# Kernel optimization log

Hardware: AMD Instinct MI355X
Metric: run time of the kernel (lower is better)

## Reference

```python
import jax, jax.numpy as jnp
import numpy as np

B, T, D_MODEL, H, D = 2, 2048, 1024, 16, 64
EPS = 1e-5


def _layernorm(x, g, b):
    m = jnp.mean(x, axis=-1, keepdims=True)
    v = jnp.var(x, axis=-1, keepdims=True)
    return (x - m) * jax.lax.rsqrt(v + EPS) * g + b


def setup_inputs() -> dict:
    key = jax.random.key(0)
    ks = jax.random.split(key, 5)
    qab = H * D
    x = jax.random.normal(ks[0], (B, T, D_MODEL), dtype=jnp.float32)
    sc = 1.0 / np.sqrt(D_MODEL)
    Wq = jax.random.normal(ks[1], (D_MODEL, qab), dtype=jnp.float32) * sc
    Wa = jax.random.normal(ks[2], (D_MODEL, qab), dtype=jnp.float32) * sc
    Wb = jax.random.normal(ks[3], (D_MODEL, qab), dtype=jnp.float32) * sc
    Wo = jax.random.normal(ks[4], (qab, D_MODEL), dtype=jnp.float32) * (1.0 / np.sqrt(qab))
    g = jnp.ones((D,), dtype=jnp.float32)
    z = jnp.zeros((D,), dtype=jnp.float32)
    return {"x": x, "Wq": Wq, "Wa": Wa, "Wb": Wb, "Wo": Wo,
            "q_gamma": g, "q_beta": z, "a_gamma": g, "a_beta": z,
            "b_gamma": g, "b_beta": z}


def reference(x, Wq, Wa, Wb, Wo, q_gamma, q_beta, a_gamma, a_beta, b_gamma, b_beta):
    def split_heads(y):  # (B,T,H*D) -> (B,H,T,D)
        Bx, Tx, _ = y.shape
        return y.reshape(Bx, Tx, H, D).transpose(0, 2, 1, 3)

    q = _layernorm(split_heads(x @ Wq), q_gamma, q_beta)
    a = _layernorm(split_heads(x @ Wa), a_gamma, a_beta)
    b = _layernorm(split_heads(x @ Wb), b_gamma, b_beta)

    # strict-exclusive cumsum of a along time
    a_excl = jnp.cumsum(a, axis=-2) - a
    # o_t = q_t . sum_{j<=t} a_excl_j (x) b_j  ==  causal (q a_excl^T) b
    scores = jnp.einsum('bhtd,bhsd->bhts', q, a_excl)  # (B,H,T,T)
    causal = jnp.tril(jnp.ones((T, T), dtype=scores.dtype))  # j <= t
    o = jnp.einsum('bhts,bhse->bhte', scores * causal, b)  # (B,H,T,D)

    o = o.transpose(0, 2, 1, 3).reshape(B, T, H * D)  # merge heads
    return o @ Wo
```

## Files before the change

kernel.cpp:

```cpp
#include <hip/hip_runtime.h>
#include <hip/hip_bf16.h>

#define T_LEN  2048
#define NHEAD  16
#define HDIM   64
#define DMODEL 1024
#define BATCH  2
#define MROWS  4096
#define L_CHK  64
#define N_CHK  (T_LEN / L_CHK)
#define BH     (BATCH * NHEAD)

typedef __attribute__((ext_vector_type(8))) short short8;
typedef __attribute__((ext_vector_type(4))) float f32x4;
typedef __attribute__((ext_vector_type(4))) unsigned short ushort4v;

#define GLDS(GP, LP) __builtin_amdgcn_global_load_lds( \
    (__attribute__((address_space(1))) void*)(void*)(GP), \
    (__attribute__((address_space(3))) void*)(LP), 16, 0, 0)

__device__ __forceinline__ unsigned short f2bf(float f) {
  union { float f; unsigned int u; } v; v.f = f;
  unsigned int r = v.u + 0x7FFFu + ((v.u >> 16) & 1u);
  return (unsigned short)(r >> 16);
}
__device__ __forceinline__ float bf2f(short s) {
  union { unsigned int u; float f; } v;
  v.u = ((unsigned int)(unsigned short)s) << 16;
  return v.f;
}

__global__ __launch_bounds__(256) void ha_convx(
    const float* __restrict__ X, short* __restrict__ Xb) {
  const size_t idx = (size_t)(blockIdx.x * 256 + threadIdx.x) * 8;
  float4 v0 = *(const float4*)(X + idx);
  float4 v1 = *(const float4*)(X + idx + 4);
  short8 o;
  o[0] = (short)f2bf(v0.x); o[1] = (short)f2bf(v0.y);
  o[2] = (short)f2bf(v0.z); o[3] = (short)f2bf(v0.w);
  o[4] = (short)f2bf(v1.x); o[5] = (short)f2bf(v1.y);
  o[6] = (short)f2bf(v1.z); o[7] = (short)f2bf(v1.w);
  *(short8*)(Xb + idx) = o;
}

__global__ __launch_bounds__(256) void ha_convT4(
    const float* __restrict__ Wq, const float* __restrict__ Wa,
    const float* __restrict__ Wb, const float* __restrict__ Wo,
    short* __restrict__ wqabT, short* __restrict__ woT) {
  __shared__ float tile[64][65];
  const int z = blockIdx.z;
  const float* W = (z == 0) ? Wq : (z == 1) ? Wa : (z == 2) ? Wb : Wo;
  short* WT = (z < 3) ? wqabT + (size_t)z * 1024 * DMODEL : woT;
  const int k0 = blockIdx.y * 64, n0 = blockIdx.x * 64;
  const int tid = threadIdx.x;
  #pragma unroll
  for (int p = 0; p < 4; ++p) {
    const int r  = p * 16 + (tid >> 4);
    const int c4 = (tid & 15) * 4;
    float4 v = *(const float4*)(W + (size_t)(k0 + r) * DMODEL + n0 + c4);
    tile[r][c4 + 0] = v.x; tile[r][c4 + 1] = v.y;
    tile[r][c4 + 2] = v.z; tile[r][c4 + 3] = v.w;
  }
  __syncthreads();
  #pragma unroll
  for (int p = 0; p < 4; ++p) {
    const int n = p * 16 + (tid >> 4);
    const int c = (tid & 15) * 4;
    ushort4v o = { f2bf(tile[c + 0][n]), f2bf(tile[c + 1][n]),
                   f2bf(tile[c + 2][n]), f2bf(tile[c + 3][n]) };
    *(ushort4v*)(WT + (size_t)(n0 + n) * DMODEL + k0 + c) = o;
  }
}

__global__ __launch_bounds__(256) void ha_gemm_qab(
    const short* __restrict__ Ab, const short* __restrict__ Bt,
    short* __restrict__ q, short* __restrict__ a, short* __restrict__ bOut,
    const float* __restrict__ qg, const float* __restrict__ qbet,
    const float* __restrict__ ag, const float* __restrict__ abet,
    const float* __restrict__ bg, const float* __restrict__ bbet) {
  __shared__ short As[128 * 32] __attribute__((aligned(16)));
  __shared__ short Bs[128 * 32] __attribute__((aligned(16)));
  const int tid = threadIdx.x;
  const int wave = tid >> 6, lane = tid & 63;
  const int m0  = blockIdx.y * 128;
  const int n0g = blockIdx.x * 128;
  short* Cbuf; const float* gamma; const float* beta;
  if (n0g < 1024)      { Cbuf = q;    gamma = qg; beta = qbet; }
  else if (n0g < 2048) { Cbuf = a;    gamma = ag; beta = abet; }
  else                 { Cbuf = bOut; gamma = bg; beta = bbet; }
  const int n0 = n0g & 1023;

  const int srow = wave * 32 + (lane >> 2);
  const int scol = (lane & 3) * 8;
  const short* agp = Ab + (size_t)(m0 + srow) * DMODEL + scol;
  const short* bgp = Bt + (size_t)(n0g + srow) * DMODEL + scol;
  short* alp = As + wave * 32 * 32;
  short* blp = Bs + wave * 32 * 32;

  f32x4 acc[4][4] = {};
  const int lm = lane & 15, kh = lane >> 4;
  const int wm = (wave >> 1) * 64, wn = (wave & 1) * 64;

  float gl[4], bl[4];
  #pragma unroll
  for (int j = 0; j < 4; ++j) {
    gl[j] = gamma[j * 16 + lm];
    bl[j] = beta[j * 16 + lm];
  }

  for (int k0 = 0; k0 < DMODEL; k0 += 32) {
    GLDS(agp,               alp);
    GLDS(agp + 16 * DMODEL, alp + 16 * 32);
    GLDS(bgp,               blp);
    GLDS(bgp + 16 * DMODEL, blp + 16 * 32);
    agp += 32; bgp += 32;
    __syncthreads();
    short8 af[4], bf[4];
    #pragma unroll
    for (int i = 0; i < 4; ++i) {
      af[i] = *(const short8*)&As[(wm + i * 16 + lm) * 32 + kh * 8];
      bf[i] = *(const short8*)&Bs[(wn + i * 16 + lm) * 32 + kh * 8];
    }
    #pragma unroll
    for (int i = 0; i < 4; ++i)
      #pragma unroll
      for (int j = 0; j < 4; ++j)
        acc[i][j] = __builtin_amdgcn_mfma_f32_16x16x32_bf16(
            af[i], bf[j], acc[i][j], 0, 0, 0);
    __syncthreads();
  }

  #pragma unroll
  for (int i = 0; i < 4; ++i) {
    float s1[4] = {0.f, 0.f, 0.f, 0.f};
    float s2[4] = {0.f, 0.f, 0.f, 0.f};
    #pragma unroll
    for (int j = 0; j < 4; ++j)
      #pragma unroll
      for (int r = 0; r < 4; ++r) {
        const float v = acc[i][j][r];
        s1[r] += v; s2[r] += v * v;
      }
    #pragma unroll
    for (int m = 1; m <= 8; m <<= 1)
      #pragma unroll
      for (int r = 0; r < 4; ++r) {
        s1[r] += __shfl_xor(s1[r], m);
        s2[r] += __shfl_xor(s2[r], m);
      }
    #pragma unroll
    for (int r = 0; r < 4; ++r) {
      const float mean = s1[r] * 0.015625f;
      const float var  = s2[r] * 0.015625f - mean * mean;
      const float rs   = rsqrtf(var + 1e-5f);
      short* cp = Cbuf + (size_t)(m0 + wm + i * 16 + kh * 4 + r) * DMODEL +
                  n0 + wn + lm;
      #pragma unroll
      for (int j = 0; j < 4; ++j)
        cp[j * 16] = (short)f2bf((acc[i][j][r] - mean) * rs * gl[j] + bl[j]);
    }
  }
}

__global__ __launch_bounds__(256) void ha_gemm_out(
    const short* __restrict__ Ab, const short* __restrict__ Bt,
    float* __restrict__ C) {
  __shared__ short As[128 * 32] __attribute__((aligned(16)));
  __shared__ short Bs[64 * 32] __attribute__((aligned(16)));
  const int tid = threadIdx.x;
  const int wave = tid >> 6, lane = tid & 63;
  const int m0 = blockIdx.y * 128;
  const int n0 = blockIdx.x * 64;

  const int arow = wave * 32 + (lane >> 2);
  const int brow = wave * 16 + (lane >> 2);
  const int scol = (lane & 3) * 8;
  const short* agp = Ab + (size_t)(m0 + arow) * DMODEL + scol;
  const short* bgp = Bt + (size_t)(n0 + brow) * DMODEL + scol;
  short* alp = As + wave * 32 * 32;
  short* blp = Bs + wave * 16 * 32;

  f32x4 acc[4][2] = {};
  const int lm = lane & 15, kh = lane >> 4;
  const int wm = (wave >> 1) * 64, wn = (wave & 1) * 32;

  for (int k0 = 0; k0 < DMODEL; k0 += 32) {
    GLDS(agp,               alp);
    GLDS(agp + 16 * DMODEL, alp + 16 * 32);
    GLDS(bgp,               blp);
    agp += 32; bgp += 32;
    __syncthreads();
    short8 af[4], bf2[2];
    #pragma unroll
    for (int i = 0; i < 4; ++i)
      af[i] = *(const short8*)&As[(wm + i * 16 + lm) * 32 + kh * 8];
    #pragma unroll
    for (int j = 0; j < 2; ++j)
      bf2[j] = *(const short8*)&Bs[(wn + j * 16 + lm) * 32 + kh * 8];
    #pragma unroll
    for (int i = 0; i < 4; ++i)
      #pragma unroll
      for (int j = 0; j < 2; ++j)
        acc[i][j] = __builtin_amdgcn_mfma_f32_16x16x32_bf16(
            af[i], bf2[j], acc[i][j], 0, 0, 0);
    __syncthreads();
  }
  #pragma unroll
  for (int i = 0; i < 4; ++i)
    #pragma unroll
    for (int j = 0; j < 2; ++j) {
      float* cp = C + (size_t)(m0 + wm + i * 16 + kh * 4) * DMODEL +
                  n0 + wn + j * 16 + lm;
      #pragma unroll
      for (int r = 0; r < 4; ++r) cp[(size_t)r * DMODEL] = acc[i][j][r];
    }
}

__global__ __launch_bounds__(256) void ha_scan1(
    const short* __restrict__ An, const short* __restrict__ Bn,
    float* __restrict__ M, float* __restrict__ Asums, float* __restrict__ Bsums) {
  __shared__ float Al[64][68];
  __shared__ float Bl[64][68];
  __shared__ float sega[4][64];
  __shared__ float segb[4][64];
  const int bid = blockIdx.x;
  const int c   = bid & (N_CHK - 1);
  const int bh  = bid >> 5;
  const int b = bh >> 4, h = bh & 15;
  const int tid = threadIdx.x;
  const size_t rowbase = ((size_t)b * T_LEN + (size_t)c * L_CHK) * DMODEL + h * HDIM;

  #pragma unroll
  for (int i = 0; i < 2; ++i) {
    const int idx = tid + 256 * i;
    const int s = idx >> 3, c8 = (idx & 7) * 8;
    short8 a8 = *(const short8*)(An + rowbase + (size_t)s * DMODEL + c8);
    short8 b8 = *(const short8*)(Bn + rowbase + (size_t)s * DMODEL + c8);
    #pragma unroll
    for (int k = 0; k < 8; ++k) {
      Al[s][c8 + k] = bf2f(a8[k]);
      Bl[s][c8 + k] = bf2f(b8[k]);
    }
  }
  __syncthreads();

  const int d = tid & 63, seg = tid >> 6;
  {
    float run = 0.f, runb = 0.f;
    for (int s = seg * 16; s < seg * 16 + 16; ++s) {
      const float va = Al[s][d];
      Al[s][d] = run;
      run  += va;
      runb += Bl[s][d];
    }
    sega[seg][d] = run;
    segb[seg][d] = runb;
  }
  __syncthreads();
  {
    float off = 0.f;
    for (int qq = 0; qq < seg; ++qq) off += sega[qq][d];
    for (int s = seg * 16; s < seg * 16 + 16; ++s) Al[s][d] += off;
    if (seg == 0) {
      Asums[((size_t)bh * N_CHK + c) * 64 + d] =
          sega[0][d] + sega[1][d] + sega[2][d] + sega[3][d];
      Bsums[((size_t)bh * N_CHK + c) * 64 + d] =
          segb[0][d] + segb[1][d] + segb[2][d] + segb[3][d];
    }
  }
  __syncthreads();

  const int e0 = (tid >> 4) * 4, d0 = (tid & 15) * 4;
  float acc[4][4];
  #pragma unroll
  for (int i = 0; i < 4; ++i)
    #pragma unroll
    for (int j = 0; j < 4; ++j) acc[i][j] = 0.f;
  #pragma unroll 8
  for (int s = 0; s < 64; ++s) {
    const float4 bv = *(const float4*)&Bl[s][e0];
    const float4 av = *(const float4*)&Al[s][d0];
    const float bb_[4] = {bv.x, bv.y, bv.z, bv.w};
    const float aa_[4] = {av.x, av.y, av.z, av.w};
    #pragma unroll
    for (int i = 0; i < 4; ++i)
      #pragma unroll
      for (int j = 0; j < 4; ++j) acc[i][j] = fmaf(bb_[i], aa_[j], acc[i][j]);
  }
  float* Mp = M + ((size_t)bh * N_CHK + c) * 4096;
  #pragma unroll
  for (int i = 0; i < 4; ++i)
    *(float4*)(Mp + (e0 + i) * 64 + d0) =
        make_float4(acc[i][0], acc[i][1], acc[i][2], acc[i][3]);
}

__global__ __launch_bounds__(64) void ha_aoff(float* __restrict__ Asums) {
  const int bh = blockIdx.x, d = threadIdx.x;
  float run = 0.f;
  for (int c = 0; c < N_CHK; ++c) {
    const size_t off = ((size_t)bh * N_CHK + c) * 64 + d;
    const float v = Asums[off];
    Asums[off] = run;
    run += v;
  }
}

__global__ __launch_bounds__(256) void ha_s2p(
    float* __restrict__ M, const float* __restrict__ Aoff,
    const float* __restrict__ Bsums) {
  const int part = blockIdx.x & 7;
  const int bh   = blockIdx.x >> 3;
  const int tid  = threadIdx.x;
  const int e = part * 8 + (tid >> 5);
  const int d = (tid & 31) * 2;
  float2 S = make_float2(0.f, 0.f);
  for (int c = 0; c < N_CHK; ++c) {
    const size_t vec = ((size_t)bh * N_CHK + c) * 64;
    const float bs = Bsums[vec + e];
    const float2 ao = *(const float2*)&Aoff[vec + d];
    float* Mp = M + ((size_t)bh * N_CHK + c) * 4096 + e * 64 + d;
    const float2 m = *(const float2*)Mp;
    *(float2*)Mp = S;
    S.x += fmaf(bs, ao.x, m.x);
    S.y += fmaf(bs, ao.y, m.y);
  }
}

__global__ __launch_bounds__(256) void ha_scan3(
    const short* __restrict__ Qn, const short* __restrict__ An,
    const short* __restrict__ Bn, const float* __restrict__ Soff,
    const float* __restrict__ Aoff, short* __restrict__ Ob) {
  __shared__ float Qt[64][68];
  __shared__ float Gt[64][68];
  __shared__ float Bl[64][68];
  __shared__ float Pt[64][68];
  const int bid = blockIdx.x;
  const int c   = bid & (N_CHK - 1);
  const int bh  = bid >> 5;
  const int b = bh >> 4, h = bh & 15;
  const int tid = threadIdx.x;
  const size_t rowbase = ((size_t)b * T_LEN + (size_t)c * L_CHK) * DMODEL + h * HDIM;

  #pragma unroll
  for (int i = 0; i < 2; ++i) {
    const int idx = tid + 256 * i;
    const int t = idx >> 3, c8 = (idx & 7) * 8;
    short8 q8 = *(const short8*)(Qn + rowbase + (size_t)t * DMODEL + c8);
    short8 a8 = *(const short8*)(An + rowbase + (size_t)t * DMODEL + c8);
    short8 b8 = *(const short8*)(Bn + rowbase + (size_t)t * DMODEL + c8);
    #pragma unroll
    for (int k = 0; k < 8; ++k) {
      Qt[c8 + k][t] = bf2f(q8[k]);
      Gt[c8 + k][t] = bf2f(a8[k]);
      Bl[t][c8 + k] = bf2f(b8[k]);
    }
  }
  __syncthreads();

  if (tid < 64) {
    float run = Aoff[((size_t)bh * N_CHK + c) * 64 + tid];
    for (int s = 0; s < 64; ++s) {
      const float v = Gt[tid][s];
      Gt[tid][s] = run;
      run += v;
    }
  }
  __syncthreads();

  const int tt = tid >> 4, ss = tid & 15;
  const int t0 = tt * 4, s0 = ss * 4;
  {
    float p[4][4];
    #pragma unroll
    for (int i = 0; i < 4; ++i)
      #pragma unroll
      for (int j = 0; j < 4; ++j) p[i][j] = 0.f;
    #pragma unroll 8
    for (int k = 0; k < 64; ++k) {
      const float4 qv = *(const float4*)&Qt[k][t0];
      const float4 gv = *(const float4*)&Gt[k][s0];
      const float qq[4] = {qv.x, qv.y, qv.z, qv.w};
      const float gg[4] = {gv.x, gv.y, gv.z, gv.w};
      #pragma unroll
      for (int i = 0; i < 4; ++i)
        #pragma unroll
        for (int j = 0; j < 4; ++j) p[i][j] = fmaf(qq[i], gg[j], p[i][j]);
    }
    #pragma unroll
    for (int i = 0; i < 4; ++i)
      #pragma unroll
      for (int j = 0; j < 4; ++j)
        Pt[s0 + j][t0 + i] = (s0 + j <= t0 + i) ? p[i][j] : 0.f;
  }
  __syncthreads();

  const float* Sg = Soff + ((size_t)bh * N_CHK + c) * 4096;
  #pragma unroll
  for (int i = 0; i < 4; ++i) {
    const int idx = tid + 256 * i;
    const int e = idx >> 4, d4 = idx & 15;
    float4 s4 = *(const float4*)(Sg + (size_t)e * 64 + d4 * 4);
    Gt[d4 * 4 + 0][e] = s4.x; Gt[d4 * 4 + 1][e] = s4.y;
    Gt[d4 * 4 + 2][e] = s4.z; Gt[d4 * 4 + 3][e] = s4.w;
  }
  __syncthreads();

  const int e0 = s0;
  float o[4][4];
  #pragma unroll
  for (int i = 0; i < 4; ++i)
    #pragma unroll
    for (int j = 0; j < 4; ++j) o[i][j] = 0.f;
  #pragma unroll 8
  for (int s = 0; s < 64; ++s) {
    const float4 pv = *(const float4*)&Pt[s][t0];
    const float4 bv = *(const float4*)&Bl[s][e0];
    const float pp[4] = {pv.x, pv.y, pv.z, pv.w};
    const float bb_[4] = {bv.x, bv.y, bv.z, bv.w};
    #pragma unroll
    for (int i = 0; i < 4; ++i)
      #pragma unroll
      for (int j = 0; j < 4; ++j) o[i][j] = fmaf(pp[i], bb_[j], o[i][j]);
  }
  #pragma unroll 8
  for (int dd = 0; dd < 64; ++dd) {
    const float4 qv = *(const float4*)&Qt[dd][t0];
    const float4 sv = *(const float4*)&Gt[dd][e0];
    const float qq[4] = {qv.x, qv.y, qv.z, qv.w};
    const float sS[4] = {sv.x, sv.y, sv.z, sv.w};
    #pragma unroll
    for (int i = 0; i < 4; ++i)
      #pragma unroll
      for (int j = 0; j < 4; ++j) o[i][j] = fmaf(qq[i], sS[j], o[i][j]);
  }
  #pragma unroll
  for (int i = 0; i < 4; ++i) {
    ushort4v o4 = { f2bf(o[i][0]), f2bf(o[i][1]), f2bf(o[i][2]), f2bf(o[i][3]) };
    *(ushort4v*)(Ob + rowbase + (size_t)(t0 + i) * DMODEL + e0) = o4;
  }
}

extern "C" void kernel_launch(void* const* d_in, const int* in_sizes, int n_in,
                              void* d_out, int out_size, void* d_ws,
                              size_t ws_size, hipStream_t stream) {
  const float* x  = (const float*)d_in[0];
  const float* Wq = (const float*)d_in[1];
  const float* Wa = (const float*)d_in[2];
  const float* Wb = (const float*)d_in[3];
  const float* Wo = (const float*)d_in[4];
  const float* qg = (const float*)d_in[5];
  const float* qb = (const float*)d_in[6];
  const float* ag = (const float*)d_in[7];
  const float* ab = (const float*)d_in[8];
  const float* bg = (const float*)d_in[9];
  const float* bb = (const float*)d_in[10];
  float* out = (float*)d_out;

  char* ws = (char*)d_ws;
  short* qn  = (short*)(ws);
  short* an  = (short*)(ws + ((size_t)8  << 20));
  short* bn  = (short*)(ws + ((size_t)16 << 20));
  short* xb  = (short*)(ws + ((size_t)24 << 20));
  short* obb = xb;
  short* wqabT = (short*)(ws + ((size_t)32 << 20));
  short* woT   = (short*)(ws + ((size_t)38 << 20));
  float* asums = (float*)(ws + ((size_t)40 << 20));
  float* bsums = asums + (size_t)BH * N_CHK * 64;
  float* Mbuf  = out;

  ha_convx<<<(MROWS * DMODEL) / (256 * 8), 256, 0, stream>>>(x, xb);
  ha_convT4<<<dim3(16, 16, 4), 256, 0, stream>>>(Wq, Wa, Wb, Wo, wqabT, woT);

  ha_gemm_qab<<<dim3(24, 32), 256, 0, stream>>>(xb, wqabT, qn, an, bn,
                                                qg, qb, ag, ab, bg, bb);

  ha_scan1<<<BH * N_CHK, 256, 0, stream>>>(an, bn, Mbuf, asums, bsums);
  ha_aoff<<<BH, 64, 0, stream>>>(asums);
  ha_s2p<<<BH * 8, 256, 0, stream>>>(Mbuf, asums, bsums);
  ha_scan3<<<BH * N_CHK, 256, 0, stream>>>(qn, an, bn, Mbuf, asums, obb);

  ha_gemm_out<<<dim3(16, 32), 256, 0, stream>>>(obb, woT, out);
}
```

Before: 205.2 us.

## Merge conversion and prefix kernels, XOR-swizzle GEMM LDS tiles

Folds the x-to-bf16 conversion into the weight-transpose launch as an extra grid slice. Folds the chunk-offset prefix scan into the state-propagation kernel: each block recomputes the prefix in LDS and one block per head writes it out. Adds an XOR swizzle to the LDS column layout of both GEMMs to cut bank conflicts on fragment reads. This removes two launches and some LDS contention, at the cost of redundant prefix work across 8 blocks per head and one extra workspace buffer.

```diff
diff --git a/kernel.cpp b/kernel.cpp
--- a/kernel.cpp
+++ b/kernel.cpp
@@ -30,29 +30,34 @@
   return v.f;
 }
 
-__global__ __launch_bounds__(256) void ha_convx(
-    const float* __restrict__ X, short* __restrict__ Xb) {
-  const size_t idx = (size_t)(blockIdx.x * 256 + threadIdx.x) * 8;
-  float4 v0 = *(const float4*)(X + idx);
-  float4 v1 = *(const float4*)(X + idx + 4);
-  short8 o;
-  o[0] = (short)f2bf(v0.x); o[1] = (short)f2bf(v0.y);
-  o[2] = (short)f2bf(v0.z); o[3] = (short)f2bf(v0.w);
-  o[4] = (short)f2bf(v1.x); o[5] = (short)f2bf(v1.y);
-  o[6] = (short)f2bf(v1.z); o[7] = (short)f2bf(v1.w);
-  *(short8*)(Xb + idx) = o;
-}
-
-__global__ __launch_bounds__(256) void ha_convT4(
+__global__ __launch_bounds__(256) void ha_conv(
     const float* __restrict__ Wq, const float* __restrict__ Wa,
     const float* __restrict__ Wb, const float* __restrict__ Wo,
-    short* __restrict__ wqabT, short* __restrict__ woT) {
+    const float* __restrict__ X,
+    short* __restrict__ wqabT, short* __restrict__ woT,
+    short* __restrict__ Xb) {
+  const int z = blockIdx.z;
+  const int tid = threadIdx.x;
+  if (z == 4) {
+    const int bidl = blockIdx.y * 16 + blockIdx.x;
+    #pragma unroll
+    for (int p = 0; p < 8; ++p) {
+      const size_t idx = (size_t)bidl * 16384 + (size_t)p * 2048 + tid * 8;
+      float4 v0 = *(const float4*)(X + idx);
+      float4 v1 = *(const float4*)(X + idx + 4);
+      short8 o;
+      o[0] = (short)f2bf(v0.x); o[1] = (short)f2bf(v0.y);
+      o[2] = (short)f2bf(v0.z); o[3] = (short)f2bf(v0.w);
+      o[4] = (short)f2bf(v1.x); o[5] = (short)f2bf(v1.y);
+      o[6] = (short)f2bf(v1.z); o[7] = (short)f2bf(v1.w);
+      *(short8*)(Xb + idx) = o;
+    }
+    return;
+  }
   __shared__ float tile[64][65];
-  const int z = blockIdx.z;
   const float* W = (z == 0) ? Wq : (z == 1) ? Wa : (z == 2) ? Wb : Wo;
   short* WT = (z < 3) ? wqabT + (size_t)z * 1024 * DMODEL : woT;
   const int k0 = blockIdx.y * 64, n0 = blockIdx.x * 64;
-  const int tid = threadIdx.x;
   #pragma unroll
   for (int p = 0; p < 4; ++p) {
     const int r  = p * 16 + (tid >> 4);
@@ -91,7 +96,7 @@
   const int n0 = n0g & 1023;
 
   const int srow = wave * 32 + (lane >> 2);
-  const int scol = (lane & 3) * 8;
+  const int scol = (((lane & 3) ^ ((lane >> 3) & 3))) * 8;
   const short* agp = Ab + (size_t)(m0 + srow) * DMODEL + scol;
   const short* bgp = Bt + (size_t)(n0g + srow) * DMODEL + scol;
   short* alp = As + wave * 32 * 32;
@@ -100,6 +105,7 @@
   f32x4 acc[4][4] = {};
   const int lm = lane & 15, kh = lane >> 4;
   const int wm = (wave >> 1) * 64, wn = (wave & 1) * 64;
+  const int khs = (kh ^ ((lm >> 1) & 3)) * 8;
 
   float gl[4], bl[4];
   #pragma unroll
@@ -118,8 +124,8 @@
     short8 af[4], bf[4];
     #pragma unroll
     for (int i = 0; i < 4; ++i) {
-      af[i] = *(const short8*)&As[(wm + i * 16 + lm) * 32 + kh * 8];
-      bf[i] = *(const short8*)&Bs[(wn + i * 16 + lm) * 32 + kh * 8];
+      af[i] = *(const short8*)&As[(wm + i * 16 + lm) * 32 + khs];
+      bf[i] = *(const short8*)&Bs[(wn + i * 16 + lm) * 32 + khs];
     }
     #pragma unroll
     for (int i = 0; i < 4; ++i)
@@ -174,7 +180,7 @@
 
   const int arow = wave * 32 + (lane >> 2);
   const int brow = wave * 16 + (lane >> 2);
-  const int scol = (lane & 3) * 8;
+  const int scol = (((lane & 3) ^ ((lane >> 3) & 3))) * 8;
   const short* agp = Ab + (size_t)(m0 + arow) * DMODEL + scol;
   const short* bgp = Bt + (size_t)(n0 + brow) * DMODEL + scol;
   short* alp = As + wave * 32 * 32;
@@ -183,6 +189,7 @@
   f32x4 acc[4][2] = {};
   const int lm = lane & 15, kh = lane >> 4;
   const int wm = (wave >> 1) * 64, wn = (wave & 1) * 32;
+  const int khs = (kh ^ ((lm >> 1) & 3)) * 8;
 
   for (int k0 = 0; k0 < DMODEL; k0 += 32) {
     GLDS(agp,               alp);
@@ -193,10 +200,10 @@
     short8 af[4], bf2[2];
     #pragma unroll
     for (int i = 0; i < 4; ++i)
-      af[i] = *(const short8*)&As[(wm + i * 16 + lm) * 32 + kh * 8];
+      af[i] = *(const short8*)&As[(wm + i * 16 + lm) * 32 + khs];
     #pragma unroll
     for (int j = 0; j < 2; ++j)
-      bf2[j] = *(const short8*)&Bs[(wn + j * 16 + lm) * 32 + kh * 8];
+      bf2[j] = *(const short8*)&Bs[(wn + j * 16 + lm) * 32 + khs];
     #pragma unroll
     for (int i = 0; i < 4; ++i)
       #pragma unroll
@@ -294,35 +301,40 @@
         make_float4(acc[i][0], acc[i][1], acc[i][2], acc[i][3]);
 }
 
-__global__ __launch_bounds__(64) void ha_aoff(float* __restrict__ Asums) {
-  const int bh = blockIdx.x, d = threadIdx.x;
-  float run = 0.f;
-  for (int c = 0; c < N_CHK; ++c) {
-    const size_t off = ((size_t)bh * N_CHK + c) * 64 + d;
-    const float v = Asums[off];
-    Asums[off] = run;
-    run += v;
-  }
-}
-
 __global__ __launch_bounds__(256) void ha_s2p(
-    float* __restrict__ M, const float* __restrict__ Aoff,
-    const float* __restrict__ Bsums) {
+    float* __restrict__ M, const float* __restrict__ Asums,
+    const float* __restrict__ Bsums, float* __restrict__ Aoff) {
+  __shared__ float ao[N_CHK][64];
   const int part = blockIdx.x & 7;
   const int bh   = blockIdx.x >> 3;
   const int tid  = threadIdx.x;
+  for (int i = tid; i < N_CHK * 64; i += 256)
+    ao[i >> 6][i & 63] = Asums[(size_t)bh * N_CHK * 64 + i];
+  __syncthreads();
+  if (tid < 64) {
+    float run = 0.f;
+    for (int c = 0; c < N_CHK; ++c) {
+      const float v = ao[c][tid];
+      ao[c][tid] = run;
+      run += v;
+    }
+  }
+  __syncthreads();
+  if (part == 0)
+    for (int i = tid; i < N_CHK * 64; i += 256)
+      Aoff[(size_t)bh * N_CHK * 64 + i] = ao[i >> 6][i & 63];
+
   const int e = part * 8 + (tid >> 5);
   const int d = (tid & 31) * 2;
   float2 S = make_float2(0.f, 0.f);
   for (int c = 0; c < N_CHK; ++c) {
-    const size_t vec = ((size_t)bh * N_CHK + c) * 64;
-    const float bs = Bsums[vec + e];
-    const float2 ao = *(const float2*)&Aoff[vec + d];
+    const float bs = Bsums[((size_t)bh * N_CHK + c) * 64 + e];
+    const float aox = ao[c][d], aoy = ao[c][d + 1];
     float* Mp = M + ((size_t)bh * N_CHK + c) * 4096 + e * 64 + d;
     const float2 m = *(const float2*)Mp;
     *(float2*)Mp = S;
-    S.x += fmaf(bs, ao.x, m.x);
-    S.y += fmaf(bs, ao.y, m.y);
+    S.x += fmaf(bs, aox, m.x);
+    S.y += fmaf(bs, aoy, m.y);
   }
 }
 
@@ -466,18 +478,18 @@
   short* woT   = (short*)(ws + ((size_t)38 << 20));
   float* asums = (float*)(ws + ((size_t)40 << 20));
   float* bsums = asums + (size_t)BH * N_CHK * 64;
+  float* aoff  = bsums + (size_t)BH * N_CHK * 64;
   float* Mbuf  = out;
 
-  ha_convx<<<(MROWS * DMODEL) / (256 * 8), 256, 0, stream>>>(x, xb);
-  ha_convT4<<<dim3(16, 16, 4), 256, 0, stream>>>(Wq, Wa, Wb, Wo, wqabT, woT);
+  ha_conv<<<dim3(16, 16, 5), 256, 0, stream>>>(Wq, Wa, Wb, Wo, x,
+                                               wqabT, woT, xb);
 
   ha_gemm_qab<<<dim3(24, 32), 256, 0, stream>>>(xb, wqabT, qn, an, bn,
                                                 qg, qb, ag, ab, bg, bb);
 
   ha_scan1<<<BH * N_CHK, 256, 0, stream>>>(an, bn, Mbuf, asums, bsums);
-  ha_aoff<<<BH, 64, 0, stream>>>(asums);
-  ha_s2p<<<BH * 8, 256, 0, stream>>>(Mbuf, asums, bsums);
-  ha_scan3<<<BH * N_CHK, 256, 0, stream>>>(qn, an, bn, Mbuf, asums, obb);
+  ha_s2p<<<BH * 8, 256, 0, stream>>>(Mbuf, asums, bsums, aoff);
+  ha_scan3<<<BH * N_CHK, 256, 0, stream>>>(qn, an, bn, Mbuf, aoff, obb);
 
   ha_gemm_out<<<dim3(16, 32), 256, 0, stream>>>(obb, woT, out);
 }
```

New measurement: 200.5 us. 1.02x faster.
